# Kernel tuning notes

Measured on AMD Instinct MI355X. Metric: run time of the kernel, lower is better.

The kernel has to match this reference:

```python
import jax, jax.numpy as jnp
import numpy as np
from jax import lax

NCLASSES = 3
NMS_PRE = 100
NMS_THR = 0.01
SCORE_THR = 0.1
MAX_NUM = 50
H, W = 248, 216
BS = 16


def make_anchors():
    # Faithful to Anchors(ranges, sizes, rotations) in __init__.
    z0s = np.array([-0.6, -0.6, -1.78], np.float32)
    sizes = np.array([[0.6, 0.8, 1.73], [0.6, 1.76, 1.73], [1.6, 3.9, 1.56]], np.float32)
    rotations = np.array([0.0, 1.57], np.float32)
    x = (np.arange(W, dtype=np.float32) + 0.5) * (69.12 / W)
    y = (np.arange(H, dtype=np.float32) + 0.5) * (79.36 / H) - 39.68
    yy, xx = np.meshgrid(y, x, indexing='ij')  # (H, W)
    anchors = np.zeros((H, W, 3, 2, 7), np.float32)
    for c in range(3):
        for r in range(2):
            anchors[:, :, c, r, 0] = xx
            anchors[:, :, c, r, 1] = yy
            anchors[:, :, c, r, 2] = z0s[c]
            anchors[:, :, c, r, 3:6] = sizes[c]
            anchors[:, :, c, r, 6] = rotations[r]
    return jnp.asarray(anchors)


def setup_inputs() -> dict:
    key = jax.random.key(0)
    k1, k2, k3 = jax.random.split(key, 3)
    return {
        'bbox_cls_pred': jax.random.normal(k1, (BS, 18, H, W), jnp.float32),
        'bbox_pred': jax.random.normal(k2, (BS, 42, H, W), jnp.float32) * 0.1,
        'bbox_dir_cls_pred': jax.random.normal(k3, (BS, 12, H, W), jnp.float32),
        'anchors': make_anchors(),
    }


def limit_period(val, offset=1.0, period=np.pi):
    return val - jnp.floor(val / period + offset) * period


def anchors2bboxes(anchors, deltas):
    xa, ya, za, wa, la, ha, ra = [anchors[:, i] for i in range(7)]
    dx, dy, dz, dw, dl, dh, dr = [deltas[:, i] for i in range(7)]
    da = jnp.sqrt(wa * wa + la * la)
    x = dx * da + xa
    y = dy * da + ya
    z = dz * ha + za + ha * 0.5
    w = wa * jnp.exp(dw)
    l = la * jnp.exp(dl)
    h = ha * jnp.exp(dh)
    z = z - h * 0.5
    theta = ra + dr
    return jnp.stack([x, y, z, w, l, h, theta], axis=-1)


def nms_keep(boxes2d, scores, valid, thresh):
    # Greedy NMS over fixed NMS_PRE boxes; invalid boxes never kept / never suppress.
    n = scores.shape[0]
    order = jnp.argsort(-jnp.where(valid, scores, -jnp.inf))
    b = boxes2d[order]
    v = valid[order]
    area = (b[:, 2] - b[:, 0]) * (b[:, 3] - b[:, 1])
    x1 = jnp.maximum(b[:, None, 0], b[None, :, 0])
    y1 = jnp.maximum(b[:, None, 1], b[None, :, 1])
    x2 = jnp.minimum(b[:, None, 2], b[None, :, 2])
    y2 = jnp.minimum(b[:, None, 3], b[None, :, 3])
    inter = jnp.maximum(x2 - x1, 0.0) * jnp.maximum(y2 - y1, 0.0)
    iou = inter / (area[:, None] + area[None, :] - inter + 1e-8)
    idx = jnp.arange(n)
    def body(i, keep):
        sup = (iou[i] > thresh) & (idx > i) & keep[i]
        return keep & ~sup
    keep = lax.fori_loop(0, n, body, v)
    return jnp.zeros(n, bool).at[order].set(keep)


def process_single(cls_pred, box_pred, dir_pred, anchors):
    # cls_pred (18,H,W), box_pred (42,H,W), dir_pred (12,H,W), anchors (H,W,3,2,7)
    cls = jnp.transpose(cls_pred, (1, 2, 0)).reshape(-1, NCLASSES)
    box = jnp.transpose(box_pred, (1, 2, 0)).reshape(-1, 7)
    dirp = jnp.transpose(dir_pred, (1, 2, 0)).reshape(-1, 2)
    anc = anchors.reshape(-1, 7)
    cls = jax.nn.sigmoid(cls)
    dir_cls = jnp.argmax(dirp, axis=1)
    _, inds = lax.top_k(jnp.max(cls, axis=1), NMS_PRE)
    cls = cls[inds]
    box = box[inds]
    dir_cls = dir_cls[inds]
    anc = anc[inds]
    bboxes = anchors2bboxes(anc, box)  # (NMS_PRE, 7): x,y,z,w,l,h,theta
    xy = bboxes[:, :2]
    wl = bboxes[:, 3:5]
    boxes2d = jnp.concatenate([xy - wl / 2, xy + wl / 2], axis=-1)
    # Torch code detaches theta through limit_period; dir term is constant.
    theta = lax.stop_gradient(limit_period(bboxes[:, 6])) + (1.0 - dir_cls.astype(bboxes.dtype)) * np.pi
    bboxes = bboxes.at[:, 6].set(theta)
    keeps = []
    for c in range(NCLASSES):
        sc = cls[:, c]
        valid = sc > SCORE_THR
        keeps.append(nms_keep(boxes2d, sc, valid, NMS_THR) & valid)
    keep = jnp.stack(keeps)            # (3, NMS_PRE)
    scores_all = cls.T                 # (3, NMS_PRE)
    flat = jnp.where(keep, scores_all, -1.0).reshape(-1)
    final_scores, fi = lax.top_k(flat, MAX_NUM)
    sel = fi % NMS_PRE
    labels = fi // NMS_PRE
    out_bboxes = bboxes[sel]
    mask = final_scores > 0.0
    return out_bboxes, labels, final_scores, mask


def reference(bbox_cls_pred, bbox_pred, bbox_dir_cls_pred, anchors):
    f = jax.vmap(process_single, in_axes=(0, 0, 0, None))
    return f(bbox_cls_pred, bbox_pred, bbox_dir_cls_pred, anchors)
```

## Files before the change

### kernel.cpp

```cpp
#include <hip/hip_runtime.h>
#include <cstdint>

#pragma clang fp contract(off)

#define HH 248
#define WW 216
#define HW (HH*WW)
#define NROW (6*HW)
#define BATCH 16
#define NPRE 100
#define MAXNUM 50
#define NB 4096
#define CAP 2048
#define CPB 4096
#define SBLK 14
#define CBLK 314
#define PIF 3.14159274101257324f

#define CNT_OFF  0
#define TB_OFF   64
#define KEYS_OFF 128
#define SH_OFF   (KEYS_OFF + BATCH*CAP*8)
#define SB_OFF   (SH_OFF + BATCH*SBLK*NB*2)

__device__ __forceinline__ float sigmoidf_ref(float x) {
    if (x >= 0.0f) {
        return 1.0f / (1.0f + expf(-x));
    } else {
        float e = expf(x);
        return e / (1.0f + e);
    }
}

__device__ __forceinline__ unsigned bucket_of(unsigned bits) {
    unsigned b = (bits >= 0x3F000000u) ? (2048u + ((bits - 0x3F000000u) >> 12))
                                       : (bits >> 19);
    return (b > (unsigned)(NB - 1)) ? (unsigned)(NB - 1) : b;
}

__global__ __launch_bounds__(256) void k_score(const float* __restrict__ cls,
                                               unsigned* __restrict__ sb,
                                               unsigned short* __restrict__ subhist) {
    int t = threadIdx.x, blk = blockIdx.x, b = blockIdx.y;
    __shared__ unsigned hist[NB];
    for (int i = t; i < NB; i += 256) hist[i] = 0;
    __syncthreads();

    const float* p = cls + (size_t)b * 18 * HW;
    unsigned* sbb = sb + (size_t)b * NROW;

    for (int k = 0; k < 4; ++k) {
        int cell0 = blk * CPB + k * 1024 + t * 4;
        if (cell0 < HW) {
            for (int a = 0; a < 6; ++a) {
                float4 l0 = *(const float4*)(p + (size_t)(a*3+0)*HW + cell0);
                float4 l1 = *(const float4*)(p + (size_t)(a*3+1)*HW + cell0);
                float4 l2 = *(const float4*)(p + (size_t)(a*3+2)*HW + cell0);
                unsigned b0 = __float_as_uint(sigmoidf_ref(fmaxf(l0.x, fmaxf(l1.x, l2.x))));
                unsigned b1 = __float_as_uint(sigmoidf_ref(fmaxf(l0.y, fmaxf(l1.y, l2.y))));
                unsigned b2 = __float_as_uint(sigmoidf_ref(fmaxf(l0.z, fmaxf(l1.z, l2.z))));
                unsigned b3 = __float_as_uint(sigmoidf_ref(fmaxf(l0.w, fmaxf(l1.w, l2.w))));
                atomicAdd(&hist[bucket_of(b0)], 1u);
                atomicAdd(&hist[bucket_of(b1)], 1u);
                atomicAdd(&hist[bucket_of(b2)], 1u);
                atomicAdd(&hist[bucket_of(b3)], 1u);
                uint4 v; v.x = b0; v.y = b1; v.z = b2; v.w = b3;
                *(uint4*)(sbb + (size_t)a*HW + cell0) = v;
            }
        }
    }
    __syncthreads();
    unsigned short* sh = subhist + (size_t)(b * SBLK + blk) * NB;
    for (int i = t; i < NB; i += 256) sh[i] = (unsigned short)hist[i];
}

__global__ __launch_bounds__(256) void k_reduce(const unsigned short* __restrict__ subhist,
                                                unsigned* __restrict__ tbo) {
    int b = blockIdx.x, t = threadIdx.x;
    __shared__ unsigned h[NB];
    __shared__ unsigned csum[256];
    const unsigned short* base = subhist + (size_t)b * SBLK * NB;
    for (int j = t; j < NB; j += 256) {
        unsigned s = 0;
        for (int k = 0; k < SBLK; ++k) s += base[(size_t)k * NB + j];
        h[j] = s;
    }
    __syncthreads();
    unsigned cs = 0;
    for (int q = 0; q < 16; ++q) cs += h[t * 16 + q];
    csum[t] = cs;
    __syncthreads();
    if (t == 0) {
        unsigned cum = 0;
        int r = 0;
        for (int u = 255; u >= 0; --u) {
            if (cum + csum[u] >= NPRE) {
                unsigned c2 = cum;
                for (int k2 = (u + 1) * 16 - 1; k2 >= u * 16; --k2) {
                    c2 += h[k2];
                    if (c2 >= NPRE) { r = k2; break; }
                }
                break;
            }
            cum += csum[u];
        }
        tbo[b] = (unsigned)r;
    }
}

__global__ __launch_bounds__(256) void k_collect(const unsigned* __restrict__ sb,
                                                 const unsigned* __restrict__ tbo,
                                                 unsigned* __restrict__ cnt,
                                                 unsigned long long* __restrict__ keys) {
    int t = threadIdx.x, blk = blockIdx.x, b = blockIdx.y;
    int i0 = blk * 1024 + t * 4;
    if (i0 >= NROW) return;
    unsigned tb = tbo[b];
    uint4 v = *(const uint4*)(sb + (size_t)b * NROW + i0);
    unsigned bs[4] = {v.x, v.y, v.z, v.w};
    for (int e = 0; e < 4; ++e) {
        unsigned bits = bs[e];
        if (bucket_of(bits) >= tb) {
            unsigned pos = atomicAdd(&cnt[b], 1u);
            if (pos < CAP) {
                int i = i0 + e;
                int a = i / HW;
                int cell = i - a * HW;
                unsigned row = (unsigned)(cell * 6 + a);
                keys[(size_t)b * CAP + pos] =
                    ((unsigned long long)bits << 32) |
                    (unsigned long long)(0xFFFFFFFFu - row);
            }
        }
    }
}

__global__ __launch_bounds__(256) void k_final(
    const float* __restrict__ cls, const float* __restrict__ box,
    const float* __restrict__ dir, const float* __restrict__ anc,
    const unsigned* __restrict__ cnt, const unsigned long long* __restrict__ keys,
    float* __restrict__ out) {
    int b = blockIdx.x, t = threadIdx.x;

    __shared__ unsigned long long keyS[CAP];
    __shared__ int   selRow[NPRE];
    __shared__ float bb[NPRE][7];
    __shared__ float b2d[NPRE][4];
    __shared__ float areaS[NPRE];
    __shared__ float clsS[3][NPRE];
    __shared__ float svalS[3][NPRE];
    __shared__ int   ordS[3][NPRE];
    __shared__ int   rankS[3][NPRE];
    __shared__ unsigned keepInit[3][4];
    __shared__ unsigned long long maskS[3][NPRE][2];
    __shared__ unsigned long long keepBits[3][2];
    __shared__ float flatS[3*NPRE];

    unsigned cn = cnt[b];
    int M = (cn < (unsigned)CAP) ? (int)cn : CAP;
    for (int i = t; i < CAP; i += 256)
        keyS[i] = (i < M) ? keys[(size_t)b * CAP + i] : 0ULL;
    __syncthreads();

    for (int i = t; i < M; i += 256) {
        unsigned long long k = keyS[i];
        int r = 0;
        for (int j = 0; j < M; ++j) r += (keyS[j] > k);
        if (r < NPRE) selRow[r] = (int)(0xFFFFFFFFu - (unsigned)(k & 0xFFFFFFFFull));
    }
    __syncthreads();

    if (t < NPRE) {
        int row = selRow[t];
        int a = row % 6;
        int cell = row / 6;
        const float* cb = cls + (size_t)b * 18 * HW + cell;
        clsS[0][t] = sigmoidf_ref(cb[(size_t)(a*3+0)*HW]);
        clsS[1][t] = sigmoidf_ref(cb[(size_t)(a*3+1)*HW]);
        clsS[2][t] = sigmoidf_ref(cb[(size_t)(a*3+2)*HW]);
        const float* db = dir + (size_t)b * 12 * HW + cell;
        float d0 = db[(size_t)(a*2+0)*HW];
        float d1 = db[(size_t)(a*2+1)*HW];
        int dircls = (d1 > d0) ? 1 : 0;
        const float* pb = box + (size_t)b * 42 * HW + cell;
        float dx = pb[(size_t)(a*7+0)*HW], dy = pb[(size_t)(a*7+1)*HW], dz = pb[(size_t)(a*7+2)*HW];
        float dw = pb[(size_t)(a*7+3)*HW], dl = pb[(size_t)(a*7+4)*HW], dh = pb[(size_t)(a*7+5)*HW];
        float dr = pb[(size_t)(a*7+6)*HW];
        const float* ab = anc + (size_t)row * 7;
        float xa = ab[0], ya = ab[1], za = ab[2];
        float wa = ab[3], la = ab[4], ha = ab[5], ra = ab[6];
        float da = sqrtf(wa*wa + la*la);
        float x = dx*da + xa;
        float y = dy*da + ya;
        float z = dz*ha + za + ha*0.5f;
        float wv = wa*expf(dw);
        float lv = la*expf(dl);
        float hv = ha*expf(dh);
        z = z - hv*0.5f;
        float th0 = ra + dr;
        float lim = th0 - floorf(th0/PIF + 1.0f)*PIF;
        float theta = lim + (1.0f - (float)dircls)*PIF;
        bb[t][0]=x; bb[t][1]=y; bb[t][2]=z; bb[t][3]=wv; bb[t][4]=lv; bb[t][5]=hv; bb[t][6]=theta;
        b2d[t][0] = x - wv*0.5f;
        b2d[t][1] = y - lv*0.5f;
        b2d[t][2] = x + wv*0.5f;
        b2d[t][3] = y + lv*0.5f;
        areaS[t] = (b2d[t][2]-b2d[t][0]) * (b2d[t][3]-b2d[t][1]);
    }
    if (t < 12) keepInit[t/4][t%4] = 0u;
    __syncthreads();

    for (int w = t; w < 3*NPRE; w += 256) {
        int c = w / NPRE, p = w % NPRE;
        float sc = clsS[c][p];
        svalS[c][p] = (sc > 0.1f) ? sc : -INFINITY;
    }
    __syncthreads();

    for (int w = t; w < 3*NPRE; w += 256) {
        int c = w / NPRE, p = w % NPRE;
        float v = svalS[c][p];
        int r = 0;
        for (int j = 0; j < NPRE; ++j) {
            float vj = svalS[c][j];
            if (vj > v || (vj == v && j < p)) ++r;
        }
        ordS[c][r] = p;
        rankS[c][p] = r;
        if (v != -INFINITY) atomicOr(&keepInit[c][r >> 5], 1u << (r & 31));
    }
    __syncthreads();

    for (int w = t; w < 3*NPRE; w += 256) {
        int c = w / NPRE, i = w % NPRE;
        int pi = ordS[c][i];
        unsigned long long m0 = 0ULL, m1 = 0ULL;
        float ax1 = b2d[pi][0], ay1 = b2d[pi][1], ax2 = b2d[pi][2], ay2 = b2d[pi][3];
        float ai = areaS[pi];
        for (int j = i + 1; j < NPRE; ++j) {
            int pj = ordS[c][j];
            float x1 = fmaxf(ax1, b2d[pj][0]);
            float y1 = fmaxf(ay1, b2d[pj][1]);
            float x2 = fminf(ax2, b2d[pj][2]);
            float y2 = fminf(ay2, b2d[pj][3]);
            float inter = fmaxf(x2 - x1, 0.0f) * fmaxf(y2 - y1, 0.0f);
            float iou = inter / (ai + areaS[pj] - inter + 1e-8f);
            if (iou > 0.01f) {
                if (j < 64) m0 |= (1ULL << j);
                else        m1 |= (1ULL << (j - 64));
            }
        }
        maskS[c][i][0] = m0;
        maskS[c][i][1] = m1;
    }
    __syncthreads();

    if (t < 3) {
        int c = t;
        unsigned long long k0 = (unsigned long long)keepInit[c][0] |
                                ((unsigned long long)keepInit[c][1] << 32);
        unsigned long long k1 = (unsigned long long)keepInit[c][2] |
                                ((unsigned long long)keepInit[c][3] << 32);
        for (int i = 0; i < NPRE; ++i) {
            unsigned long long bit = (i < 64) ? (k0 >> i) : (k1 >> (i - 64));
            if (bit & 1ULL) {
                k0 &= ~maskS[c][i][0];
                k1 &= ~maskS[c][i][1];
            }
        }
        keepBits[c][0] = k0;
        keepBits[c][1] = k1;
    }
    __syncthreads();

    for (int w = t; w < 3*NPRE; w += 256) {
        int c = w / NPRE, p = w % NPRE;
        int r = rankS[c][p];
        unsigned long long bit = (r < 64) ? (keepBits[c][0] >> r) : (keepBits[c][1] >> (r - 64));
        flatS[w] = (bit & 1ULL) ? clsS[c][p] : -1.0f;
    }
    __syncthreads();

    for (int i = t; i < 3*NPRE; i += 256) {
        float vi = flatS[i];
        int r2 = 0;
        for (int j = 0; j < 3*NPRE; ++j) {
            float vj = flatS[j];
            if (vj > vi || (vj == vi && j < i)) ++r2;
        }
        if (r2 < MAXNUM) {
            int p = i % NPRE;
            int lab = i / NPRE;
            int o = b * MAXNUM + r2;
            float* ob = out + (size_t)o * 7;
            for (int j = 0; j < 7; ++j) ob[j] = bb[p][j];
            out[BATCH*MAXNUM*7 + o] = (float)lab;
            out[BATCH*MAXNUM*8 + o] = vi;
            out[BATCH*MAXNUM*9 + o] = (vi > 0.0f) ? 1.0f : 0.0f;
        }
    }
}

extern "C" void kernel_launch(void* const* d_in, const int* in_sizes, int n_in,
                              void* d_out, int out_size, void* d_ws, size_t ws_size,
                              hipStream_t stream) {
    const float* cls = (const float*)d_in[0];
    const float* box = (const float*)d_in[1];
    const float* dir = (const float*)d_in[2];
    const float* anc = (const float*)d_in[3];
    float* out = (float*)d_out;
    char* ws = (char*)d_ws;

    unsigned* cnt = (unsigned*)(ws + CNT_OFF);
    unsigned* tb  = (unsigned*)(ws + TB_OFF);
    unsigned long long* keys = (unsigned long long*)(ws + KEYS_OFF);
    unsigned short* subhist  = (unsigned short*)(ws + SH_OFF);
    unsigned* sb             = (unsigned*)(ws + SB_OFF);

    hipMemsetAsync(cnt, 0, 64, stream);

    dim3 gs(SBLK, BATCH);
    dim3 gc(CBLK, BATCH);
    k_score  <<<gs, 256, 0, stream>>>(cls, sb, subhist);
    k_reduce <<<BATCH, 256, 0, stream>>>(subhist, tb);
    k_collect<<<gc, 256, 0, stream>>>(sb, tb, cnt, keys);
    k_final  <<<BATCH, 256, 0, stream>>>(cls, box, dir, anc, cnt, keys, out);
}
```

Before: 352.7 us.

## Recompute max-sigmoid scores in collect pass instead of storing intermediate buffer

The score pass no longer writes the per-anchor sigmoid bits to a workspace buffer. The collect pass re-reads the class logits and recomputes the max-sigmoid values, so it reads 18 floats per cell instead of 6 stored words. The score kernel now runs one 1024-cell chunk per block (more blocks) and clears the counter itself, which removes the memset launch. k_final also skips zero-filling unused key slots. The trade is more input reads and duplicated exp work in exchange for removing a large write-then-read of the intermediate buffer.

```diff
diff --git a/kernel.cpp b/kernel.cpp
--- a/kernel.cpp
+++ b/kernel.cpp
@@ -12,16 +12,13 @@
 #define MAXNUM 50
 #define NB 4096
 #define CAP 2048
-#define CPB 4096
-#define SBLK 14
-#define CBLK 314
+#define SBLK 53
 #define PIF 3.14159274101257324f
 
 #define CNT_OFF  0
 #define TB_OFF   64
 #define KEYS_OFF 128
 #define SH_OFF   (KEYS_OFF + BATCH*CAP*8)
-#define SB_OFF   (SH_OFF + BATCH*SBLK*NB*2)
 
 __device__ __forceinline__ float sigmoidf_ref(float x) {
     if (x >= 0.0f) {
@@ -39,34 +36,29 @@
 }
 
 __global__ __launch_bounds__(256) void k_score(const float* __restrict__ cls,
-                                               unsigned* __restrict__ sb,
-                                               unsigned short* __restrict__ subhist) {
+                                               unsigned short* __restrict__ subhist,
+                                               unsigned* __restrict__ cnt) {
     int t = threadIdx.x, blk = blockIdx.x, b = blockIdx.y;
     __shared__ unsigned hist[NB];
     for (int i = t; i < NB; i += 256) hist[i] = 0;
-    __syncthreads();
-
-    const float* p = cls + (size_t)b * 18 * HW;
-    unsigned* sbb = sb + (size_t)b * NROW;
-
-    for (int k = 0; k < 4; ++k) {
-        int cell0 = blk * CPB + k * 1024 + t * 4;
-        if (cell0 < HW) {
-            for (int a = 0; a < 6; ++a) {
-                float4 l0 = *(const float4*)(p + (size_t)(a*3+0)*HW + cell0);
-                float4 l1 = *(const float4*)(p + (size_t)(a*3+1)*HW + cell0);
-                float4 l2 = *(const float4*)(p + (size_t)(a*3+2)*HW + cell0);
-                unsigned b0 = __float_as_uint(sigmoidf_ref(fmaxf(l0.x, fmaxf(l1.x, l2.x))));
-                unsigned b1 = __float_as_uint(sigmoidf_ref(fmaxf(l0.y, fmaxf(l1.y, l2.y))));
-                unsigned b2 = __float_as_uint(sigmoidf_ref(fmaxf(l0.z, fmaxf(l1.z, l2.z))));
-                unsigned b3 = __float_as_uint(sigmoidf_ref(fmaxf(l0.w, fmaxf(l1.w, l2.w))));
-                atomicAdd(&hist[bucket_of(b0)], 1u);
-                atomicAdd(&hist[bucket_of(b1)], 1u);
-                atomicAdd(&hist[bucket_of(b2)], 1u);
-                atomicAdd(&hist[bucket_of(b3)], 1u);
-                uint4 v; v.x = b0; v.y = b1; v.z = b2; v.w = b3;
-                *(uint4*)(sbb + (size_t)a*HW + cell0) = v;
-            }
+    if (blk == 0 && t == 0) cnt[b] = 0;
+    __syncthreads();
+
+    int cell0 = blk * 1024 + t * 4;
+    if (cell0 < HW) {
+        const float* p = cls + (size_t)b * 18 * HW;
+        for (int a = 0; a < 6; ++a) {
+            float4 l0 = *(const float4*)(p + (size_t)(a*3+0)*HW + cell0);
+            float4 l1 = *(const float4*)(p + (size_t)(a*3+1)*HW + cell0);
+            float4 l2 = *(const float4*)(p + (size_t)(a*3+2)*HW + cell0);
+            unsigned b0 = __float_as_uint(sigmoidf_ref(fmaxf(l0.x, fmaxf(l1.x, l2.x))));
+            unsigned b1 = __float_as_uint(sigmoidf_ref(fmaxf(l0.y, fmaxf(l1.y, l2.y))));
+            unsigned b2 = __float_as_uint(sigmoidf_ref(fmaxf(l0.z, fmaxf(l1.z, l2.z))));
+            unsigned b3 = __float_as_uint(sigmoidf_ref(fmaxf(l0.w, fmaxf(l1.w, l2.w))));
+            atomicAdd(&hist[bucket_of(b0)], 1u);
+            atomicAdd(&hist[bucket_of(b1)], 1u);
+            atomicAdd(&hist[bucket_of(b2)], 1u);
+            atomicAdd(&hist[bucket_of(b3)], 1u);
         }
     }
     __syncthreads();
@@ -108,28 +100,34 @@
     }
 }
 
-__global__ __launch_bounds__(256) void k_collect(const unsigned* __restrict__ sb,
+__global__ __launch_bounds__(256) void k_collect(const float* __restrict__ cls,
                                                  const unsigned* __restrict__ tbo,
                                                  unsigned* __restrict__ cnt,
                                                  unsigned long long* __restrict__ keys) {
     int t = threadIdx.x, blk = blockIdx.x, b = blockIdx.y;
-    int i0 = blk * 1024 + t * 4;
-    if (i0 >= NROW) return;
+    int cell0 = blk * 1024 + t * 4;
+    if (cell0 >= HW) return;
     unsigned tb = tbo[b];
-    uint4 v = *(const uint4*)(sb + (size_t)b * NROW + i0);
-    unsigned bs[4] = {v.x, v.y, v.z, v.w};
-    for (int e = 0; e < 4; ++e) {
-        unsigned bits = bs[e];
-        if (bucket_of(bits) >= tb) {
-            unsigned pos = atomicAdd(&cnt[b], 1u);
-            if (pos < CAP) {
-                int i = i0 + e;
-                int a = i / HW;
-                int cell = i - a * HW;
-                unsigned row = (unsigned)(cell * 6 + a);
-                keys[(size_t)b * CAP + pos] =
-                    ((unsigned long long)bits << 32) |
-                    (unsigned long long)(0xFFFFFFFFu - row);
+    const float* p = cls + (size_t)b * 18 * HW;
+    for (int a = 0; a < 6; ++a) {
+        float4 l0 = *(const float4*)(p + (size_t)(a*3+0)*HW + cell0);
+        float4 l1 = *(const float4*)(p + (size_t)(a*3+1)*HW + cell0);
+        float4 l2 = *(const float4*)(p + (size_t)(a*3+2)*HW + cell0);
+        unsigned bs[4];
+        bs[0] = __float_as_uint(sigmoidf_ref(fmaxf(l0.x, fmaxf(l1.x, l2.x))));
+        bs[1] = __float_as_uint(sigmoidf_ref(fmaxf(l0.y, fmaxf(l1.y, l2.y))));
+        bs[2] = __float_as_uint(sigmoidf_ref(fmaxf(l0.z, fmaxf(l1.z, l2.z))));
+        bs[3] = __float_as_uint(sigmoidf_ref(fmaxf(l0.w, fmaxf(l1.w, l2.w))));
+        for (int e = 0; e < 4; ++e) {
+            unsigned bits = bs[e];
+            if (bucket_of(bits) >= tb) {
+                unsigned pos = atomicAdd(&cnt[b], 1u);
+                if (pos < CAP) {
+                    unsigned row = (unsigned)((cell0 + e) * 6 + a);
+                    keys[(size_t)b * CAP + pos] =
+                        ((unsigned long long)bits << 32) |
+                        (unsigned long long)(0xFFFFFFFFu - row);
+                }
             }
         }
     }
@@ -158,8 +156,8 @@
 
     unsigned cn = cnt[b];
     int M = (cn < (unsigned)CAP) ? (int)cn : CAP;
-    for (int i = t; i < CAP; i += 256)
-        keyS[i] = (i < M) ? keys[(size_t)b * CAP + i] : 0ULL;
+    for (int i = t; i < M; i += 256)
+        keyS[i] = keys[(size_t)b * CAP + i];
     __syncthreads();
 
     for (int i = t; i < M; i += 256) {
@@ -315,14 +313,10 @@
     unsigned* tb  = (unsigned*)(ws + TB_OFF);
     unsigned long long* keys = (unsigned long long*)(ws + KEYS_OFF);
     unsigned short* subhist  = (unsigned short*)(ws + SH_OFF);
-    unsigned* sb             = (unsigned*)(ws + SB_OFF);
-
-    hipMemsetAsync(cnt, 0, 64, stream);
-
-    dim3 gs(SBLK, BATCH);
-    dim3 gc(CBLK, BATCH);
-    k_score  <<<gs, 256, 0, stream>>>(cls, sb, subhist);
+
+    dim3 g(SBLK, BATCH);
+    k_score  <<<g, 256, 0, stream>>>(cls, subhist, cnt);
     k_reduce <<<BATCH, 256, 0, stream>>>(subhist, tb);
-    k_collect<<<gc, 256, 0, stream>>>(sb, tb, cnt, keys);
+    k_collect<<<g, 256, 0, stream>>>(cls, tb, cnt, keys);
     k_final  <<<BATCH, 256, 0, stream>>>(cls, box, dir, anc, cnt, keys, out);
 }
```

Result: faster. 326.8 us (-7.3%).
